# Performance work log

Measured on AMD Instinct MI355X. Metric: run time of the kernel, lower is better.

Reference implementation:

```python
import jax, jax.numpy as jnp
import numpy as np


def setup_inputs() -> dict:
    key = jax.random.key(0)
    k1, k2, k3 = jax.random.split(key, 3)
    B, C, H, W = 16, 512, 64, 64
    K = 32
    std = 1.0 / (K * C) ** 0.5
    x = jax.random.normal(k1, (B, C, H, W), dtype=jnp.float32)
    codewords = jax.random.uniform(k2, (K, C), dtype=jnp.float32, minval=-std, maxval=std)
    scale = jax.random.uniform(k3, (K,), dtype=jnp.float32, minval=-1.0, maxval=0.0)
    return {"x": x, "codewords": codewords, "scale": scale}


def reference(x, codewords, scale):
    # x: [B, C, H, W] -> tokens [B, N, C] with N = H*W
    B, C, H, W = x.shape
    xf = x.reshape(B, C, H * W).transpose(0, 2, 1)  # [B, N, C]

    # (avoids materializing the [B, N, K, C] tensor the torch code builds)
    x_sq = jnp.sum(xf * xf, axis=-1)                 # [B, N]
    c_sq = jnp.sum(codewords * codewords, axis=-1)   # [K]
    xc = jnp.einsum('bnc,kc->bnk', xf, codewords)    # [B, N, K]
    scaled_l2 = scale * (x_sq[..., None] - 2.0 * xc + c_sq)  # [B, N, K]

    w = jax.nn.softmax(scaled_l2, axis=2)            # [B, N, K]

    # aggregate: sum_n w[b,n,k] * (x[b,n,:] - c[k,:])
    #          = einsum(w, x) - (sum_n w) * c
    enc = jnp.einsum('bnk,bnc->bkc', w, xf) - jnp.sum(w, axis=1)[..., None] * codewords
    return enc  # [B, K, C]
```

## Files before the change

### kernel.cpp

```cpp
#include <hip/hip_runtime.h>


#define B_ 16
#define C_ 512
#define N_ 4096
#define K_ 32
#define CWS 520
#define WLS 40

typedef __attribute__((ext_vector_type(8))) short short8;
typedef __attribute__((ext_vector_type(16))) float floatx16;

__device__ inline unsigned short f2bf(float f) {
    union { float f; unsigned u; } v; v.f = f;
    unsigned r = v.u + 0x7FFFu + ((v.u >> 16) & 1u);
    return (unsigned short)(r >> 16);
}
__device__ inline float bf2f(unsigned short s) {
    union { unsigned u; float f; } v; v.u = ((unsigned)s) << 16;
    return v.f;
}

template <int USE_WS>
__global__ __launch_bounds__(256, 3)
void enc_kernel(const float* __restrict__ x, const float* __restrict__ cw,
                const float* __restrict__ scale, float* __restrict__ outp)
{
    __shared__ unsigned short cwT[K_ * CWS];
    __shared__ unsigned short Wl[4][K_ * WLS];
    __shared__ float csq[K_];
    __shared__ float scl[K_];

    const int tid  = threadIdx.x;
    const int wave = tid >> 6;
    const int lane = tid & 63;
    const int l31  = lane & 31;
    const int lh   = lane >> 5;

    const int b     = blockIdx.x >> 5;
    const int chunk = blockIdx.x & 31;
    const float* xb = x + (long)b * C_ * N_;

    if (tid < K_) scl[tid] = scale[tid];
    {
        const int k = tid >> 3, p = tid & 7;
        const float4* src = (const float4*)(cw + k * C_ + p * 64);
        float s = 0.f;
        #pragma unroll
        for (int i = 0; i < 16; ++i) {
            const float4 v = src[i];
            s += v.x*v.x + v.y*v.y + v.z*v.z + v.w*v.w;
            const unsigned lo = (unsigned)f2bf(v.x) | ((unsigned)f2bf(v.y) << 16);
            const unsigned hi = (unsigned)f2bf(v.z) | ((unsigned)f2bf(v.w) << 16);
            *(uint2*)&cwT[k * CWS + p * 64 + i * 4] = make_uint2(lo, hi);
        }
        s += __shfl_xor(s, 1); s += __shfl_xor(s, 2); s += __shfl_xor(s, 4);
        if (p == 0) csq[k] = s;
    }
    __syncthreads();

    const int n0 = chunk * 128 + wave * 32;
    const float* xg = xb + n0 + l31;

    floatx16 S;
    #pragma unroll
    for (int i = 0; i < 16; ++i) S[i] = 0.f;
    float xsq = 0.f;

    #pragma unroll
    for (int sp = 0; sp < 16; ++sp) {
        float xv[16];
        #pragma unroll
        for (int u = 0; u < 16; ++u) {
            const int c = sp * 32 + (u >> 3) * 16 + lh * 8 + (u & 7);
            xv[u] = xg[(long)c * N_];
        }
        #pragma unroll
        for (int h = 0; h < 2; ++h) {
            const int s = sp * 2 + h;
            const short8 af = *(const short8*)&cwT[l31 * CWS + s * 16 + lh * 8];
            short8 bx;
            #pragma unroll
            for (int j = 0; j < 8; ++j) {
                const float v = xv[h * 8 + j];
                xsq += v * v;
                bx[j] = (short)f2bf(v);
            }
            S = __builtin_amdgcn_mfma_f32_32x32x16_bf16(af, bx, S, 0, 0, 0);
        }
    }
    xsq += __shfl_xor(xsq, 32);

    {
        float L[16], mx = -3.4e38f;
        #pragma unroll
        for (int r = 0; r < 16; ++r) {
            const int k = (r & 3) + 8 * (r >> 2) + 4 * lh;
            L[r] = scl[k] * (xsq - 2.f * S[r] + csq[k]);
            mx = fmaxf(mx, L[r]);
        }
        mx = fmaxf(mx, __shfl_xor(mx, 32));
        float sum = 0.f;
        #pragma unroll
        for (int r = 0; r < 16; ++r) { L[r] = __expf(L[r] - mx); sum += L[r]; }
        sum += __shfl_xor(sum, 32);
        const float inv = 1.f / sum;
        #pragma unroll
        for (int r = 0; r < 16; ++r) {
            const int k = (r & 3) + 8 * (r >> 2) + 4 * lh;
            Wl[wave][k * WLS + l31] = f2bf(L[r] * inv);
        }
    }
    __syncthreads();

    short8 aw[8];
    #pragma unroll
    for (int st = 0; st < 8; ++st)
        aw[st] = *(const short8*)&Wl[st >> 1][l31 * WLS + (st & 1) * 16 + lh * 8];

    floatx16 wacc;
    #pragma unroll
    for (int i = 0; i < 16; ++i) wacc[i] = 0.f;
    {
        short8 ones;
        #pragma unroll
        for (int j = 0; j < 8; ++j) ones[j] = (short)0x3F80;
        #pragma unroll
        for (int st = 0; st < 8; ++st)
            wacc = __builtin_amdgcn_mfma_f32_32x32x16_bf16(aw[st], ones, wacc, 0, 0, 0);
    }

    float* dst = USE_WS ? (outp + (size_t)blockIdx.x * K_ * C_)
                        : (outp + (size_t)b * K_ * C_);

    #pragma unroll
    for (int t = 0; t < 4; ++t) {
        const int c = wave * 128 + t * 32 + l31;
        const float* xgc = xb + (long)c * N_ + chunk * 128 + lh * 8;
        floatx16 acc;
        #pragma unroll
        for (int i = 0; i < 16; ++i) acc[i] = 0.f;
        #pragma unroll
        for (int st = 0; st < 8; ++st) {
            const int noff = (st >> 1) * 32 + (st & 1) * 16;
            const float4 v0 = *(const float4*)(xgc + noff);
            const float4 v1 = *(const float4*)(xgc + noff + 4);
            short8 bx;
            bx[0] = (short)f2bf(v0.x); bx[1] = (short)f2bf(v0.y);
            bx[2] = (short)f2bf(v0.z); bx[3] = (short)f2bf(v0.w);
            bx[4] = (short)f2bf(v1.x); bx[5] = (short)f2bf(v1.y);
            bx[6] = (short)f2bf(v1.z); bx[7] = (short)f2bf(v1.w);
            acc = __builtin_amdgcn_mfma_f32_32x32x16_bf16(aw[st], bx, acc, 0, 0, 0);
        }
        #pragma unroll
        for (int r = 0; r < 16; ++r) {
            const int k = (r & 3) + 8 * (r >> 2) + 4 * lh;
            const float cwv = bf2f(cwT[k * CWS + c]);
            const float val = acc[r] - wacc[r] * cwv;
            if (USE_WS) dst[k * C_ + c] = val;
            else        atomicAdd(dst + k * C_ + c, val);
        }
    }
}

__global__ __launch_bounds__(256)
void reduce_kernel(const float4* __restrict__ part, float4* __restrict__ out)
{
    const int gid = blockIdx.x * 256 + threadIdx.x;
    const int bb  = gid >> 12;
    const int i4  = gid & 4095;
    const float4* p = part + ((size_t)bb * 32) * 4096 + i4;
    float4 s = make_float4(0.f, 0.f, 0.f, 0.f);
    #pragma unroll
    for (int ch = 0; ch < 32; ++ch) {
        const float4 v = p[(size_t)ch * 4096];
        s.x += v.x; s.y += v.y; s.z += v.z; s.w += v.w;
    }
    out[gid] = s;
}

extern "C" void kernel_launch(void* const* d_in, const int* in_sizes, int n_in,
                              void* d_out, int out_size, void* d_ws, size_t ws_size,
                              hipStream_t stream) {
    const float* x     = (const float*)d_in[0];
    const float* cw    = (const float*)d_in[1];
    const float* scale = (const float*)d_in[2];
    float* out = (float*)d_out;

    const size_t ws_need = (size_t)512 * K_ * C_ * sizeof(float);
    if (ws_size >= ws_need) {
        float* part = (float*)d_ws;
        hipLaunchKernelGGL(enc_kernel<1>, dim3(B_ * 32), dim3(256), 0, stream,
                           x, cw, scale, part);
        hipLaunchKernelGGL(reduce_kernel, dim3(256), dim3(256), 0, stream,
                           (const float4*)part, (float4*)out);
    } else {
        hipMemsetAsync(out, 0, (size_t)out_size * sizeof(float), stream);
        hipLaunchKernelGGL(enc_kernel<0>, dim3(B_ * 32), dim3(256), 0, stream,
                           x, cw, scale, out);
    }
}
```

Before: 218.4 us.

## Software-pipeline global x loads in both GEMM phases with register ring buffers

Issues the first x loads for the distance GEMM before the codeword staging and sync, then keeps three stages of x in flight through a register ring buffer. The second GEMM phase prefetches six float4-pair stages ahead, issuing them before the barrier, and holds all four accumulators live. This hides global load latency behind MFMA and conversion work. It costs many more VGPRs, so launch bounds drop occupancy from 3 to 2 blocks per CU.

```diff
diff --git a/kernel.cpp b/kernel.cpp
--- a/kernel.cpp
+++ b/kernel.cpp
@@ -22,7 +22,7 @@
 }
 
 template <int USE_WS>
-__global__ __launch_bounds__(256, 3)
+__global__ __launch_bounds__(256, 2)
 void enc_kernel(const float* __restrict__ x, const float* __restrict__ cw,
                 const float* __restrict__ scale, float* __restrict__ outp)
 {
@@ -41,6 +41,17 @@
     const int chunk = blockIdx.x & 31;
     const float* xb = x + (long)b * C_ * N_;
 
+    const int n0 = chunk * 128 + wave * 32;
+    const float* xg = xb + n0 + l31;
+    float xv[3][16];
+#define G1LOAD(st_, sp_)                                                       \
+    { _Pragma("unroll")                                                        \
+      for (int u = 0; u < 16; ++u)                                             \
+          xv[st_][u] = xg[(long)((sp_) * 32 + (u >> 3) * 16 + lh * 8 + (u & 7)) * N_]; }
+    G1LOAD(0, 0)
+    G1LOAD(1, 1)
+    G1LOAD(2, 2)
+
     if (tid < K_) scl[tid] = scale[tid];
     {
         const int k = tid >> 3, p = tid & 7;
@@ -59,9 +70,6 @@
     }
     __syncthreads();
 
-    const int n0 = chunk * 128 + wave * 32;
-    const float* xg = xb + n0 + l31;
-
     floatx16 S;
     #pragma unroll
     for (int i = 0; i < 16; ++i) S[i] = 0.f;
@@ -69,12 +77,7 @@
 
     #pragma unroll
     for (int sp = 0; sp < 16; ++sp) {
-        float xv[16];
-        #pragma unroll
-        for (int u = 0; u < 16; ++u) {
-            const int c = sp * 32 + (u >> 3) * 16 + lh * 8 + (u & 7);
-            xv[u] = xg[(long)c * N_];
-        }
+        const int st = sp % 3;
         #pragma unroll
         for (int h = 0; h < 2; ++h) {
             const int s = sp * 2 + h;
@@ -82,12 +85,13 @@
             short8 bx;
             #pragma unroll
             for (int j = 0; j < 8; ++j) {
-                const float v = xv[h * 8 + j];
+                const float v = xv[st][h * 8 + j];
                 xsq += v * v;
                 bx[j] = (short)f2bf(v);
             }
             S = __builtin_amdgcn_mfma_f32_32x32x16_bf16(af, bx, S, 0, 0, 0);
         }
+        if (sp + 3 < 16) G1LOAD(st, sp + 3)
     }
     xsq += __shfl_xor(xsq, 32);
 
@@ -111,6 +115,22 @@
             Wl[wave][k * WLS + l31] = f2bf(L[r] * inv);
         }
     }
+
+    float4 bv[6][2];
+#define G2LOAD(bi_, i_)                                                        \
+    { const int t_ = (i_) >> 3, st_ = (i_) & 7;                                \
+      const int c_ = wave * 128 + t_ * 32 + l31;                               \
+      const int no_ = (st_ >> 1) * 32 + (st_ & 1) * 16 + lh * 8;               \
+      const float* p_ = xb + (long)c_ * N_ + chunk * 128 + no_;                \
+      bv[bi_][0] = *(const float4*)p_;                                         \
+      bv[bi_][1] = *(const float4*)(p_ + 4); }
+    G2LOAD(0, 0)
+    G2LOAD(1, 1)
+    G2LOAD(2, 2)
+    G2LOAD(3, 3)
+    G2LOAD(4, 4)
+    G2LOAD(5, 5)
+
     __syncthreads();
 
     short8 aw[8];
@@ -130,33 +150,37 @@
             wacc = __builtin_amdgcn_mfma_f32_32x32x16_bf16(aw[st], ones, wacc, 0, 0, 0);
     }
 
+    floatx16 acc[4];
+    #pragma unroll
+    for (int t = 0; t < 4; ++t)
+        #pragma unroll
+        for (int i = 0; i < 16; ++i) acc[t][i] = 0.f;
+
+    #pragma unroll
+    for (int i = 0; i < 32; ++i) {
+        const int bi = i % 6;
+        const int t  = i >> 3, st = i & 7;
+        const float4 v0 = bv[bi][0];
+        const float4 v1 = bv[bi][1];
+        short8 bx;
+        bx[0] = (short)f2bf(v0.x); bx[1] = (short)f2bf(v0.y);
+        bx[2] = (short)f2bf(v0.z); bx[3] = (short)f2bf(v0.w);
+        bx[4] = (short)f2bf(v1.x); bx[5] = (short)f2bf(v1.y);
+        bx[6] = (short)f2bf(v1.z); bx[7] = (short)f2bf(v1.w);
+        acc[t] = __builtin_amdgcn_mfma_f32_32x32x16_bf16(aw[st], bx, acc[t], 0, 0, 0);
+        if (i + 6 < 32) G2LOAD(bi, i + 6)
+    }
+
     float* dst = USE_WS ? (outp + (size_t)blockIdx.x * K_ * C_)
                         : (outp + (size_t)b * K_ * C_);
-
     #pragma unroll
     for (int t = 0; t < 4; ++t) {
         const int c = wave * 128 + t * 32 + l31;
-        const float* xgc = xb + (long)c * N_ + chunk * 128 + lh * 8;
-        floatx16 acc;
-        #pragma unroll
-        for (int i = 0; i < 16; ++i) acc[i] = 0.f;
-        #pragma unroll
-        for (int st = 0; st < 8; ++st) {
-            const int noff = (st >> 1) * 32 + (st & 1) * 16;
-            const float4 v0 = *(const float4*)(xgc + noff);
-            const float4 v1 = *(const float4*)(xgc + noff + 4);
-            short8 bx;
-            bx[0] = (short)f2bf(v0.x); bx[1] = (short)f2bf(v0.y);
-            bx[2] = (short)f2bf(v0.z); bx[3] = (short)f2bf(v0.w);
-            bx[4] = (short)f2bf(v1.x); bx[5] = (short)f2bf(v1.y);
-            bx[6] = (short)f2bf(v1.z); bx[7] = (short)f2bf(v1.w);
-            acc = __builtin_amdgcn_mfma_f32_32x32x16_bf16(aw[st], bx, acc, 0, 0, 0);
-        }
         #pragma unroll
         for (int r = 0; r < 16; ++r) {
             const int k = (r & 3) + 8 * (r >> 2) + 4 * lh;
             const float cwv = bf2f(cwT[k * CWS + c]);
-            const float val = acc[r] - wacc[r] * cwv;
+            const float val = acc[t][r] - wacc[r] * cwv;
             if (USE_WS) dst[k * C_ + c] = val;
             else        atomicAdd(dst + k * C_ + c, val);
         }
```

Result: no change. 217.0 us (-0.7%).
